# Kernel optimization log

Hardware: AMD Instinct MI355X
Metric: run time of the kernel (lower is better)

The kernel has to match this reference:

```python
import jax, jax.numpy as jnp
import numpy as np
from jax import lax

L, D, H, MLP, P, IMG = 12, 768, 12, 3072, 16, 512
N_TOK = (IMG // P) ** 2 + 1  # 1025
HD = D // H


def setup_inputs() -> dict:
    key = jax.random.key(0)
    kit = iter(jax.random.split(key, 64))

    def rn(shape, s=0.02):
        return (jax.random.normal(next(kit), shape, jnp.float32) * s)

    inp = {
        "x": jax.random.normal(next(kit), (4, 3, IMG, IMG), jnp.float32),
        "conv_w": rn((D, 3, P, P)), "conv_b": jnp.zeros((D,), jnp.float32),
        "cls_token": rn((1, 1, D)), "pos_emb": rn((1, N_TOK, D)),
        # stacked per-block params [L, ...]
        "blk_ln1_g": jnp.ones((L, D), jnp.float32), "blk_ln1_b": jnp.zeros((L, D), jnp.float32),
        "blk_wq": rn((L, D, D)), "blk_bq": jnp.zeros((L, D), jnp.float32),
        "blk_wk": rn((L, D, D)), "blk_bk": jnp.zeros((L, D), jnp.float32),
        "blk_wv": rn((L, D, D)), "blk_bv": jnp.zeros((L, D), jnp.float32),
        "blk_wo": rn((L, D, D)), "blk_bo": jnp.zeros((L, D), jnp.float32),
        "blk_ln2_g": jnp.ones((L, D), jnp.float32), "blk_ln2_b": jnp.zeros((L, D), jnp.float32),
        "blk_w1": rn((L, D, MLP)), "blk_b1": jnp.zeros((L, MLP), jnp.float32),
        "blk_w2": rn((L, MLP, D)), "blk_b2": jnp.zeros((L, D), jnp.float32),
        # cross-attention
        "cwq": rn((D, D)), "cbq": jnp.zeros((D,), jnp.float32),
        "cwk": rn((D, D)), "cbk": jnp.zeros((D,), jnp.float32),
        "cwv": rn((D, D)), "cbv": jnp.zeros((D,), jnp.float32),
        "cwo": rn((D, D)), "cbo": jnp.zeros((D,), jnp.float32),
        # heads
        "fh_w1": rn((D, D // 2)), "fh_b1": jnp.zeros((D // 2,), jnp.float32),
        "fh_w2": rn((D // 2, 2)), "fh_b2": jnp.zeros((2,), jnp.float32),
        "vh_w1": rn((D, D // 2)), "vh_b1": jnp.zeros((D // 2,), jnp.float32),
        "vh_w2": rn((D // 2, 4)), "vh_b2": jnp.zeros((4,), jnp.float32),
        "ch_w1": rn((D, D // 2)), "ch_b1": jnp.zeros((D // 2,), jnp.float32),
        "ch_w2": rn((D // 2, 3)), "ch_b2": jnp.zeros((3,), jnp.float32),
    }
    return inp


def _ln(h, g, b):
    m = h.mean(-1, keepdims=True)
    v = ((h - m) ** 2).mean(-1, keepdims=True)
    return (h - m) / jnp.sqrt(v + 1e-5) * g + b


def _mha(qin, kvin, wq, bq, wk, bk, wv, bv, wo, bo):
    B, S, _ = qin.shape
    q = (qin @ wq + bq).reshape(B, S, H, HD).transpose(0, 2, 1, 3)
    k = (kvin @ wk + bk).reshape(B, S, H, HD).transpose(0, 2, 1, 3)
    v = (kvin @ wv + bv).reshape(B, S, H, HD).transpose(0, 2, 1, 3)
    scores = jnp.einsum('bhqd,bhkd->bhqk', q, k) / np.sqrt(HD).astype(np.float32)
    a = jax.nn.softmax(scores, axis=-1)  # full [B,H,S,S] materialized, as in source
    ctx = jnp.einsum('bhqk,bhkd->bhqd', a, v).transpose(0, 2, 1, 3).reshape(B, S, D)
    return ctx @ wo + bo


def _gelu(h):
    return jax.nn.gelu(h, approximate=False)


def reference(x, conv_w, conv_b, cls_token, pos_emb,
              blk_ln1_g, blk_ln1_b, blk_wq, blk_bq, blk_wk, blk_bk, blk_wv, blk_bv,
              blk_wo, blk_bo, blk_ln2_g, blk_ln2_b, blk_w1, blk_b1, blk_w2, blk_b2,
              cwq, cbq, cwk, cbk, cwv, cbv, cwo, cbo,
              fh_w1, fh_b1, fh_w2, fh_b2, vh_w1, vh_b1, vh_w2, vh_b2,
              ch_w1, ch_b1, ch_w2, ch_b2):
    B = x.shape[0]
    # patch embedding: Conv2d(3,D,16,16) then flatten -> [B, N, D]
    p = lax.conv_general_dilated(x, conv_w, (P, P), 'VALID',
                                 dimension_numbers=('NCHW', 'OIHW', 'NCHW'))
    p = p + conv_b[None, :, None, None]
    tok = p.reshape(B, D, -1).transpose(0, 2, 1)
    tok = jnp.concatenate([jnp.broadcast_to(cls_token, (B, 1, D)), tok], axis=1) + pos_emb

    def block(h, prm):
        g1, b1n, wq, bq, wk, bk, wv, bv, wo, bo, g2, b2n, w1, bb1, w2, bb2 = prm
        hn = _ln(h, g1, b1n)
        h = h + _mha(hn, hn, wq, bq, wk, bk, wv, bv, wo, bo)
        m = _ln(h, g2, b2n)
        h = h + (_gelu(m @ w1 + bb1) @ w2 + bb2)
        return h, None

    feats, _ = lax.scan(block, tok,
                        (blk_ln1_g, blk_ln1_b, blk_wq, blk_bq, blk_wk, blk_bk,
                         blk_wv, blk_bv, blk_wo, blk_bo, blk_ln2_g, blk_ln2_b,
                         blk_w1, blk_b1, blk_w2, blk_b2))

    # cross-attention: query=vein feats, key/value=fascia feats (both == feats)
    vf = _mha(feats, feats, cwq, cbq, cwk, cbk, cwv, cbv, cwo, cbo)

    fascia_logits = _gelu(feats @ fh_w1 + fh_b1) @ fh_w2 + fh_b2
    vein_logits = _gelu(vf @ vh_w1 + vh_b1) @ vh_w2 + vh_b2
    classification_logits = _gelu(vf @ ch_w1 + ch_b1) @ ch_w2 + ch_b2
    return (fascia_logits, vein_logits, classification_logits, feats)
```

## Files before the change

### kernel.cpp

```cpp
#include <hip/hip_runtime.h>


#define SP 1088

typedef __attribute__((ext_vector_type(8))) short short8;
typedef __attribute__((ext_vector_type(4))) short s16x4;
typedef __attribute__((ext_vector_type(4))) float floatx4;

#define EPI_BF16  0
#define EPI_BIAS  1
#define EPI_QKV   2
#define EPI_RES   3
#define EPI_GELU  4
#define EPI_PATCH 5

__device__ __forceinline__ short f2bf(float f) {
    union { float f; unsigned u; } x; x.f = f;
    return (short)((x.u + 0x7fffu + ((x.u >> 16) & 1u)) >> 16);
}
__device__ __forceinline__ float bf2f(short s) {
    union { unsigned u; float f; } x; x.u = ((unsigned)(unsigned short)s) << 16;
    return x.f;
}
__device__ __forceinline__ float gelu_f(float x) {
    return 0.5f * x * (1.f + erff(x * 0.70710678118654752f));
}
__device__ __forceinline__ void gload_lds16(const void* g, void* l) {
    __builtin_amdgcn_global_load_lds((const __attribute__((address_space(1))) void*)g,
                                     (__attribute__((address_space(3))) void*)l, 16, 0, 0);
}

template<int BN, int EPI>
__global__ __launch_bounds__(256)
void gemm_bt(const short* __restrict__ A, int lda,
             const short* __restrict__ Bt, int ldb, int K,
             short* __restrict__ O, int ldo,
             const float* __restrict__ bias0, const float* __restrict__ bias1,
             const float* __restrict__ bias2, float* __restrict__ hres,
             const float* __restrict__ pos,
             short* __restrict__ kout, short* __restrict__ vout)
{
    constexpr int BCH = BN / 64;
    constexpr int WNS = (BN == 128) ? 64 : 32;
    constexpr int NJ  = WNS / 16;
    __shared__ __align__(16) short As[2][128 * 32];
    __shared__ __align__(16) short Bs[2][BN * 32];

    const int tid = threadIdx.x;
    const int m0 = blockIdx.x * 128, n0 = blockIdx.y * BN;
    const int wave = tid >> 6, lane = tid & 63;
    const int quad = lane >> 4, l15 = lane & 15;
    const int wm = wave >> 1, wn = wave & 1;
    const int srow = tid >> 2, scol = (tid & 3) * 8;

    const short* Ag = A + (long)(m0 + srow) * lda + scol;
    const short* Bg = Bt + (long)(n0 + srow) * ldb + scol;

    const int NIT = K >> 5;
    short8 ra[2][2], rb[2][BCH];
    #pragma unroll
    for (int pp = 0; pp < 2; pp++) {
        #pragma unroll
        for (int c = 0; c < 2; c++)
            ra[pp][c] = *(const short8*)(Ag + (long)(64 * c) * lda + pp * 32);
        #pragma unroll
        for (int c = 0; c < BCH; c++)
            rb[pp][c] = *(const short8*)(Bg + (long)(64 * c) * ldb + pp * 32);
    }

    floatx4 acc[4][NJ];
    #pragma unroll
    for (int i = 0; i < 4; i++)
        #pragma unroll
        for (int j = 0; j < NJ; j++)
            acc[i][j] = floatx4{0.f, 0.f, 0.f, 0.f};

    auto step = [&](int it, int pp) {
        short* as = As[pp];
        short* bs = Bs[pp];
        #pragma unroll
        for (int c = 0; c < 2; c++)
            *(short8*)&as[(srow + 64 * c) * 32 + scol] = ra[pp][c];
        #pragma unroll
        for (int c = 0; c < BCH; c++)
            *(short8*)&bs[(srow + 64 * c) * 32 + scol] = rb[pp][c];
        __syncthreads();
        if (it + 2 < NIT) {
            const int k0 = (it + 2) * 32;
            #pragma unroll
            for (int c = 0; c < 2; c++)
                ra[pp][c] = *(const short8*)(Ag + (long)(64 * c) * lda + k0);
            #pragma unroll
            for (int c = 0; c < BCH; c++)
                rb[pp][c] = *(const short8*)(Bg + (long)(64 * c) * ldb + k0);
        }
        short8 af[4], bfrag[NJ];
        #pragma unroll
        for (int i = 0; i < 4; i++)
            af[i] = *(const short8*)&as[(wm * 64 + i * 16 + l15) * 32 + quad * 8];
        #pragma unroll
        for (int j = 0; j < NJ; j++)
            bfrag[j] = *(const short8*)&bs[(wn * WNS + j * 16 + l15) * 32 + quad * 8];
        #pragma unroll
        for (int i = 0; i < 4; i++)
            #pragma unroll
            for (int j = 0; j < NJ; j++)
                acc[i][j] = __builtin_amdgcn_mfma_f32_16x16x32_bf16(bfrag[j], af[i], acc[i][j], 0, 0, 0);
    };

    #pragma unroll 1
    for (int it = 0; it < NIT; it += 2) {
        step(it, 0);
        step(it + 1, 1);
    }

    const int mb = m0 + wm * 64 + l15;
    const int nbase = n0 + wn * WNS + quad * 4;
    #pragma unroll
    for (int i = 0; i < 4; i++) {
        const int m = mb + i * 16;
        #pragma unroll
        for (int j = 0; j < NJ; j++) {
            const int n = nbase + j * 16;
            floatx4 c4 = acc[i][j];
            if constexpr (EPI == EPI_BF16) {
                s16x4 s;
                #pragma unroll
                for (int r = 0; r < 4; r++) s[r] = f2bf(c4[r]);
                *(s16x4*)(O + (long)m * ldo + n) = s;
            } else if constexpr (EPI == EPI_BIAS) {
                floatx4 bv = *(const floatx4*)(bias0 + n);
                s16x4 s;
                #pragma unroll
                for (int r = 0; r < 4; r++) s[r] = f2bf(c4[r] + bv[r]);
                *(s16x4*)(O + (long)m * ldo + n) = s;
            } else if constexpr (EPI == EPI_QKV) {
                if (n < 768) {
                    floatx4 bv = *(const floatx4*)(bias0 + n);
                    s16x4 s;
                    #pragma unroll
                    for (int r = 0; r < 4; r++) s[r] = f2bf((c4[r] + bv[r]) * 0.125f);
                    *(s16x4*)(O + (long)m * 768 + n) = s;
                } else if (n < 1536) {
                    floatx4 bv = *(const floatx4*)(bias1 + (n - 768));
                    s16x4 s;
                    #pragma unroll
                    for (int r = 0; r < 4; r++) s[r] = f2bf(c4[r] + bv[r]);
                    *(s16x4*)(kout + (long)m * 768 + (n - 768)) = s;
                } else {
                    floatx4 bv = *(const floatx4*)(bias2 + (n - 1536));
                    s16x4 s;
                    #pragma unroll
                    for (int r = 0; r < 4; r++) s[r] = f2bf(c4[r] + bv[r]);
                    *(s16x4*)(vout + (long)m * 768 + (n - 1536)) = s;
                }
            } else if constexpr (EPI == EPI_RES) {
                floatx4 bv = *(const floatx4*)(bias0 + n);
                floatx4* hp = (floatx4*)(hres + (long)m * 768 + n);
                floatx4 hv = *hp;
                #pragma unroll
                for (int r = 0; r < 4; r++) hv[r] += c4[r] + bv[r];
                *hp = hv;
            } else if constexpr (EPI == EPI_GELU) {
                floatx4 bv = *(const floatx4*)(bias0 + n);
                s16x4 s;
                #pragma unroll
                for (int r = 0; r < 4; r++) s[r] = f2bf(gelu_f(c4[r] + bv[r]));
                *(s16x4*)(O + (long)m * ldo + n) = s;
            } else if constexpr (EPI == EPI_PATCH) {
                const int tok = m % SP;
                floatx4 v = floatx4{0.f, 0.f, 0.f, 0.f};
                if (tok >= 1 && tok < 1025) {
                    floatx4 bv = *(const floatx4*)(bias0 + n);
                    floatx4 pv = *(const floatx4*)(pos + (long)tok * 768 + n);
                    #pragma unroll
                    for (int r = 0; r < 4; r++) v[r] = c4[r] + bv[r] + pv[r];
                }
                *(floatx4*)(hres + (long)m * 768 + n) = v;
            }
        }
    }
}

__global__ __launch_bounds__(256)
void flash_attn(const short* __restrict__ qb, const short* __restrict__ kb,
                const short* __restrict__ vt, short* __restrict__ ctx)
{
    __shared__ __align__(16) short Ks[2][4096];
    __shared__ __align__(16) short Vs[2][4096];
    __shared__ __align__(16) short Ps[4][1280];

    const int tid = threadIdx.x;
    const int wave = tid >> 6, lane = tid & 63;
    const int quad = lane >> 4, l15 = lane & 15;
    const int bh = blockIdx.y, b = bh / 12, hh = bh - b * 12;
    const int q0 = blockIdx.x * 64;

    const long krow0 = (long)(b * SP) * 768 + hh * 64;
    const long vrow0 = (long)(bh * 64) * SP;
    const int srow = tid >> 2, scol8 = tid & 3;

    short8 qa[2];
    {
        const int qrow = b * SP + q0 + wave * 16 + l15;
        const short* qp = qb + (long)qrow * 768 + hh * 64 + quad * 8;
        qa[0] = *(const short8*)qp;
        qa[1] = *(const short8*)(qp + 32);
    }

    floatx4 acco[4];
    #pragma unroll
    for (int j = 0; j < 4; j++) acco[j] = floatx4{0.f, 0.f, 0.f, 0.f};
    float m_i[4], l_i[4];
    #pragma unroll
    for (int r = 0; r < 4; r++) { m_i[r] = -1e30f; l_i[r] = 0.f; }

    auto stage = [&](int kt, int buf) {
        #pragma unroll
        for (int it = 0; it < 2; it++) {
            const short* kg = kb + krow0 + (long)(kt * 64 + srow) * 768 + it * 32 + scol8 * 8;
            gload_lds16(kg, (char*)&Ks[buf][0] + (it * 256 + wave * 64) * 16);
            const short* vg = vt + vrow0 + (long)srow * SP + kt * 64 + it * 32 + scol8 * 8;
            gload_lds16(vg, (char*)&Vs[buf][0] + (it * 256 + wave * 64) * 16);
        }
    };

    stage(0, 0);
    for (int kt = 0; kt < 17; kt++) {
        const int cur = kt & 1;
        __syncthreads();
        if (kt + 1 < 17) stage(kt + 1, cur ^ 1);

        floatx4 accs[4];
        #pragma unroll
        for (int j = 0; j < 4; j++) accs[j] = floatx4{0.f, 0.f, 0.f, 0.f};
        #pragma unroll
        for (int c = 0; c < 2; c++)
            #pragma unroll
            for (int j = 0; j < 4; j++) {
                short8 kf = *(const short8*)&Ks[cur][c * 2048 + (j * 16 + l15) * 32 + quad * 8];
                accs[j] = __builtin_amdgcn_mfma_f32_16x16x32_bf16(qa[c], kf, accs[j], 0, 0, 0);
            }
        if (kt == 16) {
            #pragma unroll
            for (int j = 0; j < 4; j++)
                if (j != 0 || l15 != 0) {
                    #pragma unroll
                    for (int r = 0; r < 4; r++) accs[j][r] = -1e30f;
                }
        }

        float alpha[4], rs[4];
        #pragma unroll
        for (int r = 0; r < 4; r++) {
            float mx = fmaxf(fmaxf(accs[0][r], accs[1][r]), fmaxf(accs[2][r], accs[3][r]));
            #pragma unroll
            for (int off = 1; off < 16; off <<= 1) mx = fmaxf(mx, __shfl_xor(mx, off, 64));
            float newm = fmaxf(m_i[r], mx);
            alpha[r] = __expf(m_i[r] - newm);
            m_i[r] = newm;
            rs[r] = 0.f;
        }
        #pragma unroll
        for (int j = 0; j < 4; j++)
            #pragma unroll
            for (int r = 0; r < 4; r++) {
                float p = __expf(accs[j][r] - m_i[r]);
                rs[r] += p;
                Ps[wave][(j >> 1) * 640 + (quad * 4 + r) * 40 + (j & 1) * 16 + l15] = f2bf(p);
            }
        #pragma unroll
        for (int r = 0; r < 4; r++) {
            float s = rs[r];
            #pragma unroll
            for (int off = 1; off < 16; off <<= 1) s += __shfl_xor(s, off, 64);
            l_i[r] = alpha[r] * l_i[r] + s;
        }
        #pragma unroll
        for (int j = 0; j < 4; j++)
            #pragma unroll
            for (int r = 0; r < 4; r++) acco[j][r] *= alpha[r];

        __syncthreads();

        #pragma unroll
        for (int c = 0; c < 2; c++) {
            short8 pa = *(const short8*)&Ps[wave][c * 640 + l15 * 40 + quad * 8];
            #pragma unroll
            for (int j = 0; j < 4; j++) {
                short8 vf = *(const short8*)&Vs[cur][c * 2048 + (j * 16 + l15) * 32 + quad * 8];
                acco[j] = __builtin_amdgcn_mfma_f32_16x16x32_bf16(pa, vf, acco[j], 0, 0, 0);
            }
        }
    }

    const int orow = b * SP + q0 + wave * 16 + quad * 4;
    #pragma unroll
    for (int r = 0; r < 4; r++) {
        float inv = 1.f / l_i[r];
        #pragma unroll
        for (int j = 0; j < 4; j++)
            ctx[(long)(orow + r) * 768 + hh * 64 + j * 16 + l15] = f2bf(acco[j][r] * inv);
    }
}

__global__ void wtrans(const float* __restrict__ in, long inls, int K, int N,
                       short* __restrict__ out, long outls, int rowoff)
{
    in  += (long)blockIdx.z * inls;
    out += (long)blockIdx.z * outls;
    const int k0 = blockIdx.x * 32, n0 = blockIdx.y * 32;
    const int tx = threadIdx.x & 31, ty = threadIdx.x >> 5;
    __shared__ float t[32][33];
    #pragma unroll
    for (int i = 0; i < 4; i++)
        t[ty + i * 8][tx] = in[(long)(k0 + ty + i * 8) * N + n0 + tx];
    __syncthreads();
    #pragma unroll
    for (int i = 0; i < 4; i++)
        out[(long)(rowoff + n0 + ty + i * 8) * K + k0 + tx] = f2bf(t[tx][ty + i * 8]);
}

__global__ void f2b_k(const float* __restrict__ in, short* __restrict__ out, long n)
{
    long gid = (long)blockIdx.x * 256 + threadIdx.x;
    if (gid < n) out[gid] = f2bf(in[gid]);
}

__global__ void patch_gather(const float* __restrict__ x, short* __restrict__ out)
{
    long gid = (long)blockIdx.x * 256 + threadIdx.x;
    int m = (int)(gid / 768), k = (int)(gid % 768);
    int b = m / SP, tok = m - b * SP;
    short v = 0;
    if (tok >= 1 && tok < 1025) {
        int pidx = tok - 1, py = pidx >> 5, px = pidx & 31;
        int c = k >> 8, rem = k & 255, ii = rem >> 4, jj = rem & 15;
        float f = x[((long)(b * 3 + c) * 512 + py * 16 + ii) * 512 + px * 16 + jj];
        v = f2bf(f);
    }
    out[gid] = v;
}

__global__ void cls_fix(const float* __restrict__ cls, const float* __restrict__ pos,
                        float* __restrict__ h)
{
    int t = blockIdx.x * 256 + threadIdx.x;
    if (t >= 4 * 768) return;
    int b = t / 768, d = t % 768;
    h[(long)b * SP * 768 + d] = cls[d] + pos[d];
}

__global__ void ln_k(const float* __restrict__ h, const float* __restrict__ g,
                     const float* __restrict__ bta, short* __restrict__ out)
{
    int row = blockIdx.x * 4 + (threadIdx.x >> 6);
    int lane = threadIdx.x & 63;
    const float* hr = h + (long)row * 768;
    float v[12], s = 0.f;
    #pragma unroll
    for (int i = 0; i < 12; i++) { v[i] = hr[i * 64 + lane]; s += v[i]; }
    #pragma unroll
    for (int o = 32; o > 0; o >>= 1) s += __shfl_xor(s, o, 64);
    float mean = s * (1.f / 768.f);
    float ss = 0.f;
    #pragma unroll
    for (int i = 0; i < 12; i++) { float d = v[i] - mean; ss += d * d; }
    #pragma unroll
    for (int o = 32; o > 0; o >>= 1) ss += __shfl_xor(ss, o, 64);
    float rstd = rsqrtf(ss * (1.f / 768.f) + 1e-5f);
    #pragma unroll
    for (int i = 0; i < 12; i++) {
        int col = i * 64 + lane;
        out[(long)row * 768 + col] = f2bf((v[i] - mean) * rstd * g[col] + bta[col]);
    }
}

__global__ void vtrans(const short* __restrict__ v, short* __restrict__ vt)
{
    int bh = blockIdx.y, b = bh / 12, hh = bh % 12;
    int s0 = blockIdx.x * 64;
    int tx = threadIdx.x & 63, ty = threadIdx.x >> 6;
    __shared__ short t[64][65];
    #pragma unroll
    for (int i = 0; i < 16; i++) {
        int sl = ty * 16 + i;
        t[sl][tx] = v[(long)(b * SP + s0 + sl) * 768 + hh * 64 + tx];
    }
    __syncthreads();
    #pragma unroll
    for (int i = 0; i < 16; i++) {
        int d = ty * 16 + i;
        vt[((long)bh * 64 + d) * SP + s0 + tx] = t[tx][d];
    }
}

__global__ void logits_k(const short* __restrict__ hid, const float* __restrict__ w2,
                         const float* __restrict__ b2, float* __restrict__ o, int NO)
{
    int row = blockIdx.x * 4 + (threadIdx.x >> 6);
    int lane = threadIdx.x & 63;
    int b = row / 1025, s = row - b * 1025;
    const short* hr = hid + (long)(b * SP + s) * 384;
    float v[6];
    #pragma unroll
    for (int i = 0; i < 6; i++) v[i] = bf2f(hr[i * 64 + lane]);
    for (int n = 0; n < NO; n++) {
        float a = 0.f;
        #pragma unroll
        for (int i = 0; i < 6; i++) a += v[i] * w2[(i * 64 + lane) * NO + n];
        #pragma unroll
        for (int off = 32; off > 0; off >>= 1) a += __shfl_xor(a, off, 64);
        if (lane == 0) o[row * NO + n] = a + b2[n];
    }
}

__global__ void feats_out(const float* __restrict__ h, float* __restrict__ o)
{
    int gid = blockIdx.x * 256 + threadIdx.x;
    if (gid >= 4 * 1025 * 192) return;
    int row = gid / 192, c4 = gid % 192;
    int b = row / 1025, s = row % 1025;
    const float4* src = (const float4*)(h + (long)(b * SP + s) * 768) + c4;
    float4* dst = (float4*)(o + (long)row * 768) + c4;
    *dst = *src;
}

extern "C" void kernel_launch(void* const* d_in, const int* in_sizes, int n_in,
                              void* d_out, int out_size, void* d_ws, size_t ws_size,
                              hipStream_t stream)
{
    const float* x       = (const float*)d_in[0];
    const float* conv_w  = (const float*)d_in[1];
    const float* conv_b  = (const float*)d_in[2];
    const float* cls_tok = (const float*)d_in[3];
    const float* pos_emb = (const float*)d_in[4];
    const float* ln1g = (const float*)d_in[5];
    const float* ln1b = (const float*)d_in[6];
    const float* wq = (const float*)d_in[7];
    const float* bq = (const float*)d_in[8];
    const float* wk = (const float*)d_in[9];
    const float* bk = (const float*)d_in[10];
    const float* wv = (const float*)d_in[11];
    const float* bv = (const float*)d_in[12];
    const float* wo = (const float*)d_in[13];
    const float* bo = (const float*)d_in[14];
    const float* ln2g = (const float*)d_in[15];
    const float* ln2b = (const float*)d_in[16];
    const float* w1 = (const float*)d_in[17];
    const float* b1 = (const float*)d_in[18];
    const float* w2 = (const float*)d_in[19];
    const float* b2 = (const float*)d_in[20];
    const float* cwq = (const float*)d_in[21];
    const float* cbq = (const float*)d_in[22];
    const float* cwk = (const float*)d_in[23];
    const float* cbk = (const float*)d_in[24];
    const float* cwv = (const float*)d_in[25];
    const float* cbv = (const float*)d_in[26];
    const float* cwo = (const float*)d_in[27];
    const float* cbo = (const float*)d_in[28];
    const float* fh_w1 = (const float*)d_in[29];
    const float* fh_b1 = (const float*)d_in[30];
    const float* fh_w2 = (const float*)d_in[31];
    const float* fh_b2 = (const float*)d_in[32];
    const float* vh_w1 = (const float*)d_in[33];
    const float* vh_b1 = (const float*)d_in[34];
    const float* vh_w2 = (const float*)d_in[35];
    const float* vh_b2 = (const float*)d_in[36];
    const float* ch_w1 = (const float*)d_in[37];
    const float* ch_b1 = (const float*)d_in[38];
    const float* ch_w2 = (const float*)d_in[39];
    const float* ch_b2 = (const float*)d_in[40];
    float* out = (float*)d_out;

    char* ws = (char*)d_ws;
    size_t off = 0;
    auto alc = [&](size_t b) { char* p = ws + off; off += (b + 255) & ~(size_t)255; return p; };
    float* h     = (float*)alc(4352L * 768 * 4);
    short* abuf  = (short*)alc(4352L * 768 * 2);
    short* gbuf  = (short*)alc(4352L * 3072 * 2);
    short* qb    = (short*)alc(4352L * 768 * 2);
    short* kb    = (short*)alc(4352L * 768 * 2);
    short* vb    = (short*)alc(4352L * 768 * 2);
    short* vt    = (short*)alc(48L * 64 * SP * 2);
    short* ctx   = (short*)alc(4352L * 768 * 2);
    short* fbuf  = (short*)alc(4352L * 768 * 2);
    short* vfbuf = (short*)alc(4352L * 768 * 2);
    short* hid   = (short*)alc(4352L * 384 * 2);
    short* wqkvT = (short*)alc(12L * 2304 * 768 * 2);
    short* woT   = (short*)alc(12L * 768 * 768 * 2);
    short* w1T   = (short*)alc(12L * 3072 * 768 * 2);
    short* w2T   = (short*)alc(12L * 768 * 3072 * 2);
    short* convT = (short*)alc(768L * 768 * 2);
    short* cqkvT = (short*)alc(2304L * 768 * 2);
    short* coT   = (short*)alc(768L * 768 * 2);
    short* fh1T  = (short*)alc(384L * 768 * 2);
    short* vh1T  = (short*)alc(384L * 768 * 2);
    short* ch1T  = (short*)alc(384L * 768 * 2);
    short* dummy = (short*)d_ws;

    wtrans<<<dim3(24, 24, 12), 256, 0, stream>>>(wq, 589824L, 768, 768, wqkvT, 1769472L, 0);
    wtrans<<<dim3(24, 24, 12), 256, 0, stream>>>(wk, 589824L, 768, 768, wqkvT, 1769472L, 768);
    wtrans<<<dim3(24, 24, 12), 256, 0, stream>>>(wv, 589824L, 768, 768, wqkvT, 1769472L, 1536);
    wtrans<<<dim3(24, 24, 12), 256, 0, stream>>>(wo, 589824L, 768, 768, woT, 589824L, 0);
    wtrans<<<dim3(24, 96, 12), 256, 0, stream>>>(w1, 2359296L, 768, 3072, w1T, 2359296L, 0);
    wtrans<<<dim3(96, 24, 12), 256, 0, stream>>>(w2, 2359296L, 3072, 768, w2T, 2359296L, 0);
    wtrans<<<dim3(24, 24, 1), 256, 0, stream>>>(cwq, 0, 768, 768, cqkvT, 0, 0);
    wtrans<<<dim3(24, 24, 1), 256, 0, stream>>>(cwk, 0, 768, 768, cqkvT, 0, 768);
    wtrans<<<dim3(24, 24, 1), 256, 0, stream>>>(cwv, 0, 768, 768, cqkvT, 0, 1536);
    wtrans<<<dim3(24, 24, 1), 256, 0, stream>>>(cwo, 0, 768, 768, coT, 0, 0);
    wtrans<<<dim3(24, 12, 1), 256, 0, stream>>>(fh_w1, 0, 768, 384, fh1T, 0, 0);
    wtrans<<<dim3(24, 12, 1), 256, 0, stream>>>(vh_w1, 0, 768, 384, vh1T, 0, 0);
    wtrans<<<dim3(24, 12, 1), 256, 0, stream>>>(ch_w1, 0, 768, 384, ch1T, 0, 0);
    f2b_k<<<2304, 256, 0, stream>>>(conv_w, convT, 589824L);

    patch_gather<<<13056, 256, 0, stream>>>(x, abuf);
    gemm_bt<64, EPI_PATCH><<<dim3(34, 12), 256, 0, stream>>>(
        abuf, 768, convT, 768, 768,
        dummy, 768, conv_b, nullptr, nullptr, h, pos_emb, nullptr, nullptr);
    cls_fix<<<12, 256, 0, stream>>>(cls_tok, pos_emb, h);

    for (int l = 0; l < 12; l++) {
        ln_k<<<1088, 256, 0, stream>>>(h, ln1g + l * 768, ln1b + l * 768, abuf);
        gemm_bt<128, EPI_QKV><<<dim3(34, 18), 256, 0, stream>>>(
            abuf, 768, wqkvT + (long)l * 2304 * 768, 768, 768,
            qb, 768, bq + l * 768, bk + l * 768, bv + l * 768,
            nullptr, nullptr, kb, vb);
        vtrans<<<dim3(17, 48), 256, 0, stream>>>(vb, vt);
        flash_attn<<<dim3(17, 48), 256, 0, stream>>>(qb, kb, vt, ctx);
        gemm_bt<64, EPI_RES><<<dim3(34, 12), 256, 0, stream>>>(
            ctx, 768, woT + (long)l * 768 * 768, 768, 768,
            dummy, 768, bo + l * 768, nullptr, nullptr, h, nullptr, nullptr, nullptr);
        ln_k<<<1088, 256, 0, stream>>>(h, ln2g + l * 768, ln2b + l * 768, abuf);
        gemm_bt<128, EPI_GELU><<<dim3(34, 24), 256, 0, stream>>>(
            abuf, 768, w1T + (long)l * 3072 * 768, 768, 768,
            gbuf, 3072, b1 + l * 3072, nullptr, nullptr, nullptr, nullptr, nullptr, nullptr);
        gemm_bt<64, EPI_RES><<<dim3(34, 12), 256, 0, stream>>>(
            gbuf, 3072, w2T + (long)l * 768 * 3072, 3072, 3072,
            dummy, 768, b2 + l * 768, nullptr, nullptr, h, nullptr, nullptr, nullptr);
    }

    f2b_k<<<13056, 256, 0, stream>>>(h, fbuf, 4352L * 768);
    gemm_bt<128, EPI_QKV><<<dim3(34, 18), 256, 0, stream>>>(
        fbuf, 768, cqkvT, 768, 768,
        qb, 768, cbq, cbk, cbv, nullptr, nullptr, kb, vb);
    vtrans<<<dim3(17, 48), 256, 0, stream>>>(vb, vt);
    flash_attn<<<dim3(17, 48), 256, 0, stream>>>(qb, kb, vt, ctx);
    gemm_bt<64, EPI_BIAS><<<dim3(34, 12), 256, 0, stream>>>(
        ctx, 768, coT, 768, 768,
        vfbuf, 768, cbo, nullptr, nullptr, nullptr, nullptr, nullptr, nullptr);

    gemm_bt<64, EPI_GELU><<<dim3(34, 6), 256, 0, stream>>>(
        fbuf, 768, fh1T, 768, 768,
        hid, 384, fh_b1, nullptr, nullptr, nullptr, nullptr, nullptr, nullptr);
    logits_k<<<1025, 256, 0, stream>>>(hid, fh_w2, fh_b2, out + 0, 2);
    gemm_bt<64, EPI_GELU><<<dim3(34, 6), 256, 0, stream>>>(
        vfbuf, 768, vh1T, 768, 768,
        hid, 384, vh_b1, nullptr, nullptr, nullptr, nullptr, nullptr, nullptr);
    logits_k<<<1025, 256, 0, stream>>>(hid, vh_w2, vh_b2, out + 8200, 4);
    gemm_bt<64, EPI_GELU><<<dim3(34, 6), 256, 0, stream>>>(
        vfbuf, 768, ch1T, 768, 768,
        hid, 384, ch_b1, nullptr, nullptr, nullptr, nullptr, nullptr, nullptr);
    logits_k<<<1025, 256, 0, stream>>>(hid, ch_w2, ch_b2, out + 24600, 3);

    feats_out<<<3075, 256, 0, stream>>>(h, out + 36900);

    (void)in_sizes; (void)n_in; (void)out_size; (void)ws_size;
}
```

Before: 3.490 ms.

## Swizzle LDS tiles, use exp2 softmax, compute row sums via MFMA

Applies an XOR swizzle to the LDS layout of GEMM and attention K/V tiles so that fragment reads avoid bank conflicts. The attention softmax switches to exp2 by folding log2(e) into the Q scale. Row sums are computed with an extra MFMA against a ones vector, which removes the shuffle reductions. The block-wide barrier before the PV step is replaced with a per-wave LDS wait, relying on each wave owning its own P buffer. The risks are a subtle race if other waves' staging overlaps, plus a small precision change from summing bf16-rounded P values.

```diff
diff --git a/kernel.cpp b/kernel.cpp
--- a/kernel.cpp
+++ b/kernel.cpp
@@ -13,6 +13,8 @@
 #define EPI_RES   3
 #define EPI_GELU  4
 #define EPI_PATCH 5
+
+#define QSCALE 0.18033688011112042f
 
 __device__ __forceinline__ short f2bf(float f) {
     union { float f; unsigned u; } x; x.f = f;
@@ -52,6 +54,8 @@
     const int quad = lane >> 4, l15 = lane & 15;
     const int wm = wave >> 1, wn = wave & 1;
     const int srow = tid >> 2, scol = (tid & 3) * 8;
+    const int sslot8 = ((tid & 3) ^ ((srow >> 1) & 3)) * 8;
+    const int rsw = (l15 >> 1) & 3;
 
     const short* Ag = A + (long)(m0 + srow) * lda + scol;
     const short* Bg = Bt + (long)(n0 + srow) * ldb + scol;
@@ -80,10 +84,10 @@
         short* bs = Bs[pp];
         #pragma unroll
         for (int c = 0; c < 2; c++)
-            *(short8*)&as[(srow + 64 * c) * 32 + scol] = ra[pp][c];
+            *(short8*)&as[(srow + 64 * c) * 32 + sslot8] = ra[pp][c];
         #pragma unroll
         for (int c = 0; c < BCH; c++)
-            *(short8*)&bs[(srow + 64 * c) * 32 + scol] = rb[pp][c];
+            *(short8*)&bs[(srow + 64 * c) * 32 + sslot8] = rb[pp][c];
         __syncthreads();
         if (it + 2 < NIT) {
             const int k0 = (it + 2) * 32;
@@ -97,10 +101,10 @@
         short8 af[4], bfrag[NJ];
         #pragma unroll
         for (int i = 0; i < 4; i++)
-            af[i] = *(const short8*)&as[(wm * 64 + i * 16 + l15) * 32 + quad * 8];
+            af[i] = *(const short8*)&as[(wm * 64 + i * 16 + l15) * 32 + (quad ^ rsw) * 8];
         #pragma unroll
         for (int j = 0; j < NJ; j++)
-            bfrag[j] = *(const short8*)&bs[(wn * WNS + j * 16 + l15) * 32 + quad * 8];
+            bfrag[j] = *(const short8*)&bs[(wn * WNS + j * 16 + l15) * 32 + (quad ^ rsw) * 8];
         #pragma unroll
         for (int i = 0; i < 4; i++)
             #pragma unroll
@@ -139,7 +143,7 @@
                     floatx4 bv = *(const floatx4*)(bias0 + n);
                     s16x4 s;
                     #pragma unroll
-                    for (int r = 0; r < 4; r++) s[r] = f2bf((c4[r] + bv[r]) * 0.125f);
+                    for (int r = 0; r < 4; r++) s[r] = f2bf((c4[r] + bv[r]) * QSCALE);
                     *(s16x4*)(O + (long)m * 768 + n) = s;
                 } else if (n < 1536) {
                     floatx4 bv = *(const floatx4*)(bias1 + (n - 768));
@@ -198,7 +202,9 @@
 
     const long krow0 = (long)(b * SP) * 768 + hh * 64;
     const long vrow0 = (long)(bh * 64) * SP;
-    const int srow = tid >> 2, scol8 = tid & 3;
+    const int srow = tid >> 2;
+    const int scol8 = (tid & 3) ^ ((srow >> 1) & 3);
+    const int rsw = (l15 >> 1) & 3;
 
     short8 qa[2];
     {
@@ -208,12 +214,16 @@
         qa[1] = *(const short8*)(qp + 32);
     }
 
+    const short ov = (l15 == 0) ? (short)0x3F80 : (short)0;
+    const short8 vones = {ov, ov, ov, ov, ov, ov, ov, ov};
+
     floatx4 acco[4];
     #pragma unroll
     for (int j = 0; j < 4; j++) acco[j] = floatx4{0.f, 0.f, 0.f, 0.f};
-    float m_i[4], l_i[4];
-    #pragma unroll
-    for (int r = 0; r < 4; r++) { m_i[r] = -1e30f; l_i[r] = 0.f; }
+    floatx4 accl = floatx4{0.f, 0.f, 0.f, 0.f};
+    float m_i[4];
+    #pragma unroll
+    for (int r = 0; r < 4; r++) m_i[r] = -1e30f;
 
     auto stage = [&](int kt, int buf) {
         #pragma unroll
@@ -238,7 +248,7 @@
         for (int c = 0; c < 2; c++)
             #pragma unroll
             for (int j = 0; j < 4; j++) {
-                short8 kf = *(const short8*)&Ks[cur][c * 2048 + (j * 16 + l15) * 32 + quad * 8];
+                short8 kf = *(const short8*)&Ks[cur][c * 2048 + (j * 16 + l15) * 32 + (quad ^ rsw) * 8];
                 accs[j] = __builtin_amdgcn_mfma_f32_16x16x32_bf16(qa[c], kf, accs[j], 0, 0, 0);
             }
         if (kt == 16) {
@@ -250,54 +260,50 @@
                 }
         }
 
-        float alpha[4], rs[4];
+        float alpha[4];
         #pragma unroll
         for (int r = 0; r < 4; r++) {
             float mx = fmaxf(fmaxf(accs[0][r], accs[1][r]), fmaxf(accs[2][r], accs[3][r]));
             #pragma unroll
             for (int off = 1; off < 16; off <<= 1) mx = fmaxf(mx, __shfl_xor(mx, off, 64));
             float newm = fmaxf(m_i[r], mx);
-            alpha[r] = __expf(m_i[r] - newm);
+            alpha[r] = exp2f(m_i[r] - newm);
             m_i[r] = newm;
-            rs[r] = 0.f;
         }
         #pragma unroll
         for (int j = 0; j < 4; j++)
             #pragma unroll
             for (int r = 0; r < 4; r++) {
-                float p = __expf(accs[j][r] - m_i[r]);
-                rs[r] += p;
+                float p = exp2f(accs[j][r] - m_i[r]);
                 Ps[wave][(j >> 1) * 640 + (quad * 4 + r) * 40 + (j & 1) * 16 + l15] = f2bf(p);
             }
         #pragma unroll
-        for (int r = 0; r < 4; r++) {
-            float s = rs[r];
-            #pragma unroll
-            for (int off = 1; off < 16; off <<= 1) s += __shfl_xor(s, off, 64);
-            l_i[r] = alpha[r] * l_i[r] + s;
-        }
-        #pragma unroll
         for (int j = 0; j < 4; j++)
             #pragma unroll
             for (int r = 0; r < 4; r++) acco[j][r] *= alpha[r];
-
-        __syncthreads();
+        #pragma unroll
+        for (int r = 0; r < 4; r++) accl[r] *= alpha[r];
+
+        asm volatile("s_waitcnt lgkmcnt(0)" ::: "memory");
+        __builtin_amdgcn_sched_barrier(0);
 
         #pragma unroll
         for (int c = 0; c < 2; c++) {
             short8 pa = *(const short8*)&Ps[wave][c * 640 + l15 * 40 + quad * 8];
             #pragma unroll
             for (int j = 0; j < 4; j++) {
-                short8 vf = *(const short8*)&Vs[cur][c * 2048 + (j * 16 + l15) * 32 + quad * 8];
+                short8 vf = *(const short8*)&Vs[cur][c * 2048 + (j * 16 + l15) * 32 + (quad ^ rsw) * 8];
                 acco[j] = __builtin_amdgcn_mfma_f32_16x16x32_bf16(pa, vf, acco[j], 0, 0, 0);
             }
+            accl = __builtin_amdgcn_mfma_f32_16x16x32_bf16(pa, vones, accl, 0, 0, 0);
         }
     }
 
     const int orow = b * SP + q0 + wave * 16 + quad * 4;
     #pragma unroll
     for (int r = 0; r < 4; r++) {
-        float inv = 1.f / l_i[r];
+        float lsum = __shfl(accl[r], (lane & 48), 64);
+        float inv = 1.f / lsum;
         #pragma unroll
         for (int j = 0; j < 4; j++)
             ctx[(long)(orow + r) * 768 + hh * 64 + j * 16 + l15] = f2bf(acco[j][r] * inv);
```

Result: faster. 3.379 ms (-3.2%).
